# Performance work log

Measured on AMD Instinct MI355X. Metric: run time of the kernel, lower is better.

## Reference

```python
import jax, jax.numpy as jnp
import numpy as np
from jax import lax

DN = ('NCHW', 'OIHW', 'NCHW')


def _conv(x, w, padding, groups=1):
    return lax.conv_general_dilated(
        x, w, window_strides=(1, 1), padding=padding,
        dimension_numbers=DN, feature_group_count=groups)


def _l2_normalize(t, axis=-1, eps=1e-12):
    # matches torch.nn.functional.normalize: x / max(||x||, eps)
    n = jnp.sqrt(jnp.sum(t * t, axis=axis, keepdims=True))
    return t / jnp.maximum(n, eps)


def _topk_masked_softmax(attn, k):
    # attn: [b, H, C, C]; keep exactly the top-k entries per row (by index,
    # matching torch.topk + scatter), set rest to -inf, then softmax.
    C = attn.shape[-1]
    idx = lax.top_k(attn, k)[1]                              # [b, H, C, k]
    mask = jax.nn.one_hot(idx, C, dtype=jnp.bool_).any(-2)   # [b, H, C, C]
    return jax.nn.softmax(jnp.where(mask, attn, -jnp.inf), axis=-1)


def setup_inputs() -> dict:
    key = jax.random.key(0)
    ks = jax.random.split(key, 4)
    dim, heads, b, h, w = 64, 2, 8, 256, 256
    x = jax.random.normal(ks[0], (b, dim, h, w), dtype=jnp.float32)
    w_qkv = jax.random.normal(ks[1], (3 * dim, dim, 1, 1), dtype=jnp.float32) * 0.05
    w_dw = jax.random.normal(ks[2], (3 * dim, 1, 3, 3), dtype=jnp.float32) * 0.05
    w_proj = jax.random.normal(ks[3], (dim, dim, 1, 1), dtype=jnp.float32) * 0.05
    temperature = jnp.ones((heads, 1, 1), dtype=jnp.float32)
    a1 = jnp.array([0.2], dtype=jnp.float32)
    a2 = jnp.array([0.2], dtype=jnp.float32)
    a3 = jnp.array([0.2], dtype=jnp.float32)
    return {"x": x, "w_qkv": w_qkv, "w_dw": w_dw, "w_proj": w_proj,
            "temperature": temperature, "a1": a1, "a2": a2, "a3": a3}


def reference(x, w_qkv, w_dw, w_proj, temperature, a1, a2, a3):
    heads = temperature.shape[0]
    b, c, h, w = x.shape
    qkv = _conv(x, w_qkv, padding=[(0, 0), (0, 0)])
    qkv = _conv(qkv, w_dw, padding=[(1, 1), (1, 1)], groups=3 * c)
    q, k, v = jnp.split(qkv, 3, axis=1)

    def to_heads(t):  # b (head C) h w -> b head C (h w)
        return t.reshape(b, heads, c // heads, h * w)

    q, k, v = to_heads(q), to_heads(k), to_heads(v)
    q = _l2_normalize(q)
    k = _l2_normalize(k)

    C = c // heads
    attn = jnp.einsum('bhcn,bhdn->bhcd', q, k) * temperature  # [b, H, C, C]

    attn1 = _topk_masked_softmax(attn, C // 2)
    attn2 = _topk_masked_softmax(attn, (C * 2) // 3)
    attn3 = _topk_masked_softmax(attn, (C * 3) // 4)

    out = (jnp.einsum('bhcd,bhdn->bhcn', attn1, v) * a1
           + jnp.einsum('bhcd,bhdn->bhcn', attn2, v) * a2
           + jnp.einsum('bhcd,bhdn->bhcn', attn3, v) * a3)

    out = out.reshape(b, c, h, w)
    return _conv(out, w_proj, padding=[(0, 0), (0, 0)])
```

## Files before the change

kernel.cpp:

```cpp
#include <hip/hip_runtime.h>
#include <math.h>

constexpr int B_   = 8;
constexpr int CIN  = 64;
constexpr int C3   = 192;
constexpr int HWID = 256;
constexpr long long NPIX = 65536;

constexpr int K3_CHUNKS = 128;
constexpr int K3_CELLS  = 1088;

constexpr size_t SZ_QKV1_1B = (size_t)C3 * NPIX;
constexpr size_t SZ_QKB_1B  = (size_t)128 * NPIX;
constexpr size_t SZ_GRAM = (size_t)B_ * 2 * 32 * 32;
constexpr size_t SZ_NORM = (size_t)B_ * 2 * 64;
constexpr size_t SZ_M    = (size_t)B_ * 64 * 64;
constexpr size_t SZ_PART = (size_t)B_ * 2 * K3_CHUNKS * K3_CELLS;

constexpr int LSTR = 68;

__global__ __launch_bounds__(256) void k1_qkv1x1(const float* __restrict__ x,
                                                 const float* __restrict__ wqkv,
                                                 float* __restrict__ qkv1, int b0) {
  __shared__ __align__(16) float xs[64][LSTR];
  __shared__ __align__(16) float Wt[64][LSTR];
  const int t = threadIdx.x;
  const int lb = blockIdx.z;
  const long long n0 = (long long)blockIdx.x * 64;
  const int oc0 = blockIdx.y * 64;
  const float* xb = x + (size_t)(b0 + lb) * CIN * NPIX;
  float* outb = qkv1 + (size_t)lb * SZ_QKV1_1B;

  {
    const int p4 = (t & 15) * 4;
#pragma unroll
    for (int r = 0; r < 4; ++r) {
      const int ic = (t >> 4) + 16 * r;
      const float4 v = *(const float4*)(xb + (size_t)ic * NPIX + n0 + p4);
      *(float4*)(&xs[ic][p4]) = v;
    }
    const int ic4 = (t & 15) * 4;
#pragma unroll
    for (int r = 0; r < 4; ++r) {
      const int ocl = (t >> 4) + 16 * r;
      const float4 w = *(const float4*)(wqkv + (size_t)(oc0 + ocl) * 64 + ic4);
      Wt[ic4 + 0][ocl] = w.x;
      Wt[ic4 + 1][ocl] = w.y;
      Wt[ic4 + 2][ocl] = w.z;
      Wt[ic4 + 3][ocl] = w.w;
    }
  }
  __syncthreads();

  const int ocl0 = (t >> 4) * 4;
  const int p0   = (t & 15) * 4;
  float acc[4][4] = {};
#pragma unroll 4
  for (int j = 0; j < 64; ++j) {
    const float4 a  = *(const float4*)(&Wt[j][ocl0]);
    const float4 bq = *(const float4*)(&xs[j][p0]);
    const float av[4] = {a.x, a.y, a.z, a.w};
    const float bv[4] = {bq.x, bq.y, bq.z, bq.w};
#pragma unroll
    for (int i = 0; i < 4; ++i)
#pragma unroll
      for (int p = 0; p < 4; ++p)
        acc[i][p] = fmaf(av[i], bv[p], acc[i][p]);
  }
#pragma unroll
  for (int i = 0; i < 4; ++i) {
    float4 o;
    o.x = acc[i][0]; o.y = acc[i][1]; o.z = acc[i][2]; o.w = acc[i][3];
    *(float4*)(outb + (size_t)(oc0 + ocl0 + i) * NPIX + n0 + p0) = o;
  }
}

__global__ __launch_bounds__(256) void k2_dwconv(const float* __restrict__ qkv1,
                                                 const float* __restrict__ wdw,
                                                 float* __restrict__ qkb,
                                                 size_t qkb_stride,
                                                 float* __restrict__ vout) {
  const int r0 = blockIdx.x * 16;
  const int ch = blockIdx.y;
  const int lb = blockIdx.z;
  const int t  = threadIdx.x;
  __shared__ __align__(16) float sm[18][256];
  const float* p = qkv1 + (size_t)lb * SZ_QKV1_1B + (size_t)ch * NPIX;

  for (int idx = t; idx < 18 * 64; idx += 256) {
    const int rr = idx >> 6;
    const int c4 = (idx & 63) * 4;
    const int gr = r0 - 1 + rr;
    float4 v = make_float4(0.f, 0.f, 0.f, 0.f);
    if (gr >= 0 && gr < HWID) v = *(const float4*)(p + (size_t)gr * HWID + c4);
    *(float4*)(&sm[rr][c4]) = v;
  }
  float w[9];
#pragma unroll
  for (int i = 0; i < 9; ++i) w[i] = wdw[ch * 9 + i];
  __syncthreads();

  const int col = t;
  const bool cl = (col > 0), cr = (col < 255);
  float l0 = cl ? sm[0][col - 1] : 0.f, m0 = sm[0][col], r0v = cr ? sm[0][col + 1] : 0.f;
  float l1 = cl ? sm[1][col - 1] : 0.f, m1 = sm[1][col], r1v = cr ? sm[1][col + 1] : 0.f;
  float* dst = (ch < 128)
                   ? (qkb + (size_t)lb * qkb_stride + (size_t)ch * NPIX)
                   : (vout + (size_t)lb * 64 * NPIX + (size_t)(ch - 128) * NPIX);
#pragma unroll
  for (int k = 0; k < 16; ++k) {
    const float l2 = cl ? sm[k + 2][col - 1] : 0.f;
    const float m2 = sm[k + 2][col];
    const float r2v = cr ? sm[k + 2][col + 1] : 0.f;
    float acc = w[0] * l0;
    acc = fmaf(w[1], m0, acc);  acc = fmaf(w[2], r0v, acc);
    acc = fmaf(w[3], l1, acc);  acc = fmaf(w[4], m1, acc);
    acc = fmaf(w[5], r1v, acc); acc = fmaf(w[6], l2, acc);
    acc = fmaf(w[7], m2, acc);  acc = fmaf(w[8], r2v, acc);
    dst[(size_t)(r0 + k) * HWID + col] = acc;
    l0 = l1; m0 = m1; r0v = r1v;
    l1 = l2; m1 = m2; r1v = r2v;
  }
}

__global__ __launch_bounds__(1024) void k3_gram(const float* __restrict__ qkbuf,
                                                size_t qkb_stride,
                                                float* __restrict__ part, int b0) {
  const int chunk = blockIdx.x;
  const int h = blockIdx.y;
  const int lb = blockIdx.z;
  const int b = b0 + lb;
  const int t = threadIdx.x;
  const int nt = t & 15;
  const int tile = t >> 4;
  const int c0 = (tile & 7) * 4;
  const int d0 = (tile >> 3) * 4;
  const bool do_qn = (d0 == 0);
  const bool do_kn = (c0 == 0);
  const float* base = qkbuf + (size_t)lb * qkb_stride;
  const float* qb = base + (size_t)(h * 32) * NPIX;
  const float* kb = base + (size_t)(64 + h * 32) * NPIX;

  float acc[4][4] = {};
  float qn[4] = {}, kn[4] = {};
  const long long n0 = (long long)chunk * 512 + nt * 4;
#pragma unroll 2
  for (int s = 0; s < 8; ++s) {
    const long long n = n0 + (long long)s * 64;
    float4 qv[4], kv[4];
#pragma unroll
    for (int i = 0; i < 4; ++i)
      qv[i] = *(const float4*)(qb + (size_t)(c0 + i) * NPIX + n);
#pragma unroll
    for (int j = 0; j < 4; ++j)
      kv[j] = *(const float4*)(kb + (size_t)(d0 + j) * NPIX + n);
#pragma unroll
    for (int i = 0; i < 4; ++i)
#pragma unroll
      for (int j = 0; j < 4; ++j) {
        float a = acc[i][j];
        a = fmaf(qv[i].x, kv[j].x, a);
        a = fmaf(qv[i].y, kv[j].y, a);
        a = fmaf(qv[i].z, kv[j].z, a);
        a = fmaf(qv[i].w, kv[j].w, a);
        acc[i][j] = a;
      }
    if (do_qn) {
#pragma unroll
      for (int i = 0; i < 4; ++i) {
        float a = qn[i];
        a = fmaf(qv[i].x, qv[i].x, a);
        a = fmaf(qv[i].y, qv[i].y, a);
        a = fmaf(qv[i].z, qv[i].z, a);
        a = fmaf(qv[i].w, qv[i].w, a);
        qn[i] = a;
      }
    }
    if (do_kn) {
#pragma unroll
      for (int j = 0; j < 4; ++j) {
        float a = kn[j];
        a = fmaf(kv[j].x, kv[j].x, a);
        a = fmaf(kv[j].y, kv[j].y, a);
        a = fmaf(kv[j].z, kv[j].z, a);
        a = fmaf(kv[j].w, kv[j].w, a);
        kn[j] = a;
      }
    }
  }

  float* pb = part + (((size_t)(b * 2 + h)) * K3_CHUNKS + chunk) * K3_CELLS;
#pragma unroll
  for (int i = 0; i < 4; ++i)
#pragma unroll
    for (int j = 0; j < 4; ++j) {
      float v = acc[i][j];
      v += __shfl_xor(v, 1); v += __shfl_xor(v, 2);
      v += __shfl_xor(v, 4); v += __shfl_xor(v, 8);
      if (nt == 0) pb[(c0 + i) * 32 + (d0 + j)] = v;
    }
  if (do_qn) {
#pragma unroll
    for (int i = 0; i < 4; ++i) {
      float v = qn[i];
      v += __shfl_xor(v, 1); v += __shfl_xor(v, 2);
      v += __shfl_xor(v, 4); v += __shfl_xor(v, 8);
      if (nt == 0) pb[1024 + c0 + i] = v;
    }
  }
  if (do_kn) {
#pragma unroll
    for (int j = 0; j < 4; ++j) {
      float v = kn[j];
      v += __shfl_xor(v, 1); v += __shfl_xor(v, 2);
      v += __shfl_xor(v, 4); v += __shfl_xor(v, 8);
      if (nt == 0) pb[1056 + d0 + j] = v;
    }
  }
}

__global__ __launch_bounds__(256) void k3_reduce(const float* __restrict__ part,
                                                 float* __restrict__ gram,
                                                 float* __restrict__ norms) {
  const int e = blockIdx.x * 256 + threadIdx.x;
  const int bh = e / K3_CELLS;
  const int cell = e - bh * K3_CELLS;
  const float* p = part + ((size_t)bh * K3_CHUNKS) * K3_CELLS + cell;
  float s0 = 0.f, s1 = 0.f;
#pragma unroll 4
  for (int ch = 0; ch < K3_CHUNKS; ch += 2) {
    s0 += p[(size_t)ch * K3_CELLS];
    s1 += p[(size_t)(ch + 1) * K3_CELLS];
  }
  const float s = s0 + s1;
  if (cell < 1024) gram[(size_t)bh * 1024 + cell] = s;
  else             norms[(size_t)bh * 64 + (cell - 1024)] = s;
}

__global__ __launch_bounds__(256) void k4_attn(const float* __restrict__ gram,
                                               const float* __restrict__ norms,
                                               const float* __restrict__ temp,
                                               const float* __restrict__ a1,
                                               const float* __restrict__ a2,
                                               const float* __restrict__ a3,
                                               const float* __restrict__ wproj,
                                               float* __restrict__ M) {
  const int b = blockIdx.x;
  const int t = threadIdx.x;
  __shared__ float A[2][32][32];
  if (t < 64) {
    const int h = t >> 5, c = t & 31;
    const float* g = gram + (((size_t)b * 2 + h) * 32 + c) * 32;
    const float* nb = norms + ((size_t)b * 2 + h) * 64;
    const float qn = fmaxf(sqrtf(nb[c]), 1e-12f);
    const float tmph = temp[h];
    float v[32];
#pragma unroll
    for (int d = 0; d < 32; ++d) {
      const float kn = fmaxf(sqrtf(nb[32 + d]), 1e-12f);
      v[d] = g[d] / (qn * kn) * tmph;
    }
    int rank[32];
#pragma unroll
    for (int i = 0; i < 32; ++i) {
      int r = 0;
#pragma unroll
      for (int j = 0; j < 32; ++j)
        r += (v[j] > v[i]) || (v[j] == v[i] && j < i);
      rank[i] = r;
    }
    float acc[32];
#pragma unroll
    for (int d = 0; d < 32; ++d) acc[d] = 0.f;
    const float aws[3] = {a1[0], a2[0], a3[0]};
    const int kvs[3] = {16, 21, 24};
#pragma unroll 1
    for (int kk = 0; kk < 3; ++kk) {
      float mx = -3.4e38f;
#pragma unroll
      for (int d = 0; d < 32; ++d)
        if (rank[d] < kvs[kk]) mx = fmaxf(mx, v[d]);
      float s = 0.f;
#pragma unroll
      for (int d = 0; d < 32; ++d)
        if (rank[d] < kvs[kk]) s += expf(v[d] - mx);
      const float inv = aws[kk] / s;
#pragma unroll
      for (int d = 0; d < 32; ++d)
        if (rank[d] < kvs[kk]) acc[d] += expf(v[d] - mx) * inv;
    }
#pragma unroll
    for (int d = 0; d < 32; ++d) A[h][c][d] = acc[d];
  }
  __syncthreads();
  for (int e = t; e < 4096; e += 256) {
    const int oc = e >> 6, j = e & 63, h = j >> 5, d = j & 31;
    float s = 0.f;
#pragma unroll
    for (int c = 0; c < 32; ++c)
      s += wproj[oc * 64 + h * 32 + c] * A[h][c][d];
    M[(size_t)b * 4096 + e] = s;
  }
}

__global__ __launch_bounds__(256) void k5_out(float* vy,
                                              const float* __restrict__ M) {
  __shared__ __align__(16) float vs[64][LSTR];
  __shared__ __align__(16) float Mt[64][LSTR];
  const int t = threadIdx.x;
  const int b = blockIdx.y;
  const long long n0 = (long long)blockIdx.x * 64;
  float* vb = vy + (size_t)b * 64 * NPIX;
  const float* Mb = M + (size_t)b * 4096;

  {
    const int p4 = (t & 15) * 4;
#pragma unroll
    for (int r = 0; r < 4; ++r) {
      const int j = (t >> 4) + 16 * r;
      const float4 v = *(const float4*)(vb + (size_t)j * NPIX + n0 + p4);
      *(float4*)(&vs[j][p4]) = v;
    }
    const int j4 = (t & 15) * 4;
#pragma unroll
    for (int r = 0; r < 4; ++r) {
      const int oc = (t >> 4) + 16 * r;
      const float4 m = *(const float4*)(Mb + (size_t)oc * 64 + j4);
      Mt[j4 + 0][oc] = m.x;
      Mt[j4 + 1][oc] = m.y;
      Mt[j4 + 2][oc] = m.z;
      Mt[j4 + 3][oc] = m.w;
    }
  }
  __syncthreads();

  const int ocl0 = (t >> 4) * 4;
  const int p0   = (t & 15) * 4;
  float acc[4][4] = {};
#pragma unroll 4
  for (int j = 0; j < 64; ++j) {
    const float4 a  = *(const float4*)(&Mt[j][ocl0]);
    const float4 bq = *(const float4*)(&vs[j][p0]);
    const float av[4] = {a.x, a.y, a.z, a.w};
    const float bv[4] = {bq.x, bq.y, bq.z, bq.w};
#pragma unroll
    for (int i = 0; i < 4; ++i)
#pragma unroll
      for (int p = 0; p < 4; ++p)
        acc[i][p] = fmaf(av[i], bv[p], acc[i][p]);
  }
#pragma unroll
  for (int i = 0; i < 4; ++i) {
    float4 o;
    o.x = acc[i][0]; o.y = acc[i][1]; o.z = acc[i][2]; o.w = acc[i][3];
    *(float4*)(vb + (size_t)(ocl0 + i) * NPIX + n0 + p0) = o;
  }
}

extern "C" void kernel_launch(void* const* d_in, const int* in_sizes, int n_in,
                              void* d_out, int out_size, void* d_ws, size_t ws_size,
                              hipStream_t stream) {
  const float* x     = (const float*)d_in[0];
  const float* wqkv  = (const float*)d_in[1];
  const float* wdw   = (const float*)d_in[2];
  const float* wproj = (const float*)d_in[3];
  const float* temp  = (const float*)d_in[4];
  const float* a1    = (const float*)d_in[5];
  const float* a2    = (const float*)d_in[6];
  const float* a3    = (const float*)d_in[7];
  float* y = (float*)d_out;
  float* ws = (float*)d_ws;

  const size_t ws_floats = ws_size / sizeof(float);
  const size_t smalls = SZ_GRAM + SZ_NORM + SZ_M + SZ_PART;
  const size_t needA = 4 * SZ_QKV1_1B + (size_t)B_ * SZ_QKB_1B + smalls;

  dim3 blk(256);
  if (ws_floats >= needA) {
    float* qkv1  = ws;
    float* qkb   = qkv1 + 4 * SZ_QKV1_1B;
    float* gram  = qkb + (size_t)B_ * SZ_QKB_1B;
    float* norms = gram + SZ_GRAM;
    float* M     = norms + SZ_NORM;
    float* part  = M + SZ_M;

    for (int half = 0; half < 2; ++half) {
      const int b0 = half * 4;
      k1_qkv1x1<<<dim3(1024, 3, 4), blk, 0, stream>>>(x, wqkv, qkv1, b0);
      k2_dwconv<<<dim3(16, C3, 4), blk, 0, stream>>>(
          qkv1, wdw, qkb + (size_t)b0 * SZ_QKB_1B, SZ_QKB_1B,
          y + (size_t)b0 * 64 * NPIX);
    }
    k3_gram<<<dim3(K3_CHUNKS, 2, B_), dim3(1024), 0, stream>>>(
        qkb, SZ_QKB_1B, part, 0);
    k3_reduce<<<dim3(68), blk, 0, stream>>>(part, gram, norms);
    k4_attn<<<dim3(B_), blk, 0, stream>>>(gram, norms, temp, a1, a2, a3, wproj, M);
    k5_out<<<dim3(1024, B_), blk, 0, stream>>>(y, M);
  } else {
    float* qkv1  = ws;
    float* qkb   = qkv1 + SZ_QKV1_1B;
    float* gram  = qkb + SZ_QKB_1B;
    float* norms = gram + SZ_GRAM;
    float* M     = norms + SZ_NORM;
    float* part  = M + SZ_M;

    for (int b = 0; b < B_; ++b) {
      k1_qkv1x1<<<dim3(1024, 3, 1), blk, 0, stream>>>(x, wqkv, qkv1, b);
      k2_dwconv<<<dim3(16, C3, 1), blk, 0, stream>>>(
          qkv1, wdw, qkb, 0, y + (size_t)b * 64 * NPIX);
      k3_gram<<<dim3(K3_CHUNKS, 2, 1), dim3(1024), 0, stream>>>(qkb, 0, part, b);
    }
    k3_reduce<<<dim3(68), blk, 0, stream>>>(part, gram, norms);
    k4_attn<<<dim3(B_), blk, 0, stream>>>(gram, norms, temp, a1, a2, a3, wproj, M);
    k5_out<<<dim3(1024, B_), blk, 0, stream>>>(y, M);
  }
}
```

Measured before the change: 761.8 us.

## Stage Gram tiles in shared memory with 8x8 register blocking and transposed partials

The Gram kernel now loads 32x256 Q and K chunks into shared memory, and each of 256 threads computes an 8x8 output tile instead of reading 4x4 tiles straight from global memory with 1024 threads. This raises arithmetic reuse per load and doubles the chunk count to 256. The partials layout is transposed to cell-major so the reduce kernel can sum each cell's 256 chunks with coalesced loads and a wavefront shuffle. The larger per-thread register tile may lower occupancy, and the partials writes are now strided.

```diff
diff --git a/kernel.cpp b/kernel.cpp
--- a/kernel.cpp
+++ b/kernel.cpp
@@ -7,7 +7,7 @@
 constexpr int HWID = 256;
 constexpr long long NPIX = 65536;
 
-constexpr int K3_CHUNKS = 128;
+constexpr int K3_CHUNKS = 256;
 constexpr int K3_CELLS  = 1088;
 
 constexpr size_t SZ_QKV1_1B = (size_t)C3 * NPIX;
@@ -15,7 +15,7 @@
 constexpr size_t SZ_GRAM = (size_t)B_ * 2 * 32 * 32;
 constexpr size_t SZ_NORM = (size_t)B_ * 2 * 64;
 constexpr size_t SZ_M    = (size_t)B_ * 64 * 64;
-constexpr size_t SZ_PART = (size_t)B_ * 2 * K3_CHUNKS * K3_CELLS;
+constexpr size_t SZ_PART = (size_t)B_ * 2 * K3_CELLS * K3_CHUNKS;
 
 constexpr int LSTR = 68;
 
@@ -123,41 +123,54 @@
   }
 }
 
-__global__ __launch_bounds__(1024) void k3_gram(const float* __restrict__ qkbuf,
-                                                size_t qkb_stride,
-                                                float* __restrict__ part, int b0) {
+__global__ __launch_bounds__(256) void k3_gram(const float* __restrict__ qkbuf,
+                                               size_t qkb_stride,
+                                               float* __restrict__ part, int b0) {
+  constexpr int LS = 260;
+  __shared__ __align__(16) float qs[32][LS];
+  __shared__ __align__(16) float ks[32][LS];
   const int chunk = blockIdx.x;
   const int h = blockIdx.y;
   const int lb = blockIdx.z;
   const int b = b0 + lb;
   const int t = threadIdx.x;
+  const float* base = qkbuf + (size_t)lb * qkb_stride;
+  const float* qg = base + (size_t)(h * 32) * NPIX + (size_t)chunk * 256;
+  const float* kg = base + (size_t)(64 + h * 32) * NPIX + (size_t)chunk * 256;
+
+  {
+    const int col4 = (t & 63) * 4;
+    const int rb = t >> 6;
+#pragma unroll
+    for (int it = 0; it < 8; ++it) {
+      const int row = it * 4 + rb;
+      *(float4*)(&qs[row][col4]) = *(const float4*)(qg + (size_t)row * NPIX + col4);
+      *(float4*)(&ks[row][col4]) = *(const float4*)(kg + (size_t)row * NPIX + col4);
+    }
+  }
+  __syncthreads();
+
   const int nt = t & 15;
   const int tile = t >> 4;
-  const int c0 = (tile & 7) * 4;
-  const int d0 = (tile >> 3) * 4;
+  const int c0 = (tile & 3) * 8;
+  const int d0 = (tile >> 2) * 8;
   const bool do_qn = (d0 == 0);
   const bool do_kn = (c0 == 0);
-  const float* base = qkbuf + (size_t)lb * qkb_stride;
-  const float* qb = base + (size_t)(h * 32) * NPIX;
-  const float* kb = base + (size_t)(64 + h * 32) * NPIX;
-
-  float acc[4][4] = {};
-  float qn[4] = {}, kn[4] = {};
-  const long long n0 = (long long)chunk * 512 + nt * 4;
-#pragma unroll 2
-  for (int s = 0; s < 8; ++s) {
-    const long long n = n0 + (long long)s * 64;
-    float4 qv[4], kv[4];
-#pragma unroll
-    for (int i = 0; i < 4; ++i)
-      qv[i] = *(const float4*)(qb + (size_t)(c0 + i) * NPIX + n);
-#pragma unroll
-    for (int j = 0; j < 4; ++j)
-      kv[j] = *(const float4*)(kb + (size_t)(d0 + j) * NPIX + n);
-#pragma unroll
-    for (int i = 0; i < 4; ++i)
-#pragma unroll
-      for (int j = 0; j < 4; ++j) {
+
+  float acc[8][8] = {};
+  float qn[8] = {}, kn[8] = {};
+#pragma unroll 1
+  for (int s = 0; s < 4; ++s) {
+    const int nn = s * 64 + nt * 4;
+    float4 qv[8], kv[8];
+#pragma unroll
+    for (int i = 0; i < 8; ++i) qv[i] = *(const float4*)(&qs[c0 + i][nn]);
+#pragma unroll
+    for (int j = 0; j < 8; ++j) kv[j] = *(const float4*)(&ks[d0 + j][nn]);
+#pragma unroll
+    for (int i = 0; i < 8; ++i)
+#pragma unroll
+      for (int j = 0; j < 8; ++j) {
         float a = acc[i][j];
         a = fmaf(qv[i].x, kv[j].x, a);
         a = fmaf(qv[i].y, kv[j].y, a);
@@ -167,7 +180,7 @@
       }
     if (do_qn) {
 #pragma unroll
-      for (int i = 0; i < 4; ++i) {
+      for (int i = 0; i < 8; ++i) {
         float a = qn[i];
         a = fmaf(qv[i].x, qv[i].x, a);
         a = fmaf(qv[i].y, qv[i].y, a);
@@ -178,7 +191,7 @@
     }
     if (do_kn) {
 #pragma unroll
-      for (int j = 0; j < 4; ++j) {
+      for (int j = 0; j < 8; ++j) {
         float a = kn[j];
         a = fmaf(kv[j].x, kv[j].x, a);
         a = fmaf(kv[j].y, kv[j].y, a);
@@ -189,32 +202,32 @@
     }
   }
 
-  float* pb = part + (((size_t)(b * 2 + h)) * K3_CHUNKS + chunk) * K3_CELLS;
-#pragma unroll
-  for (int i = 0; i < 4; ++i)
-#pragma unroll
-    for (int j = 0; j < 4; ++j) {
+  float* pb = part + ((size_t)(b * 2 + h) * K3_CELLS) * K3_CHUNKS + chunk;
+#pragma unroll
+  for (int i = 0; i < 8; ++i)
+#pragma unroll
+    for (int j = 0; j < 8; ++j) {
       float v = acc[i][j];
       v += __shfl_xor(v, 1); v += __shfl_xor(v, 2);
       v += __shfl_xor(v, 4); v += __shfl_xor(v, 8);
-      if (nt == 0) pb[(c0 + i) * 32 + (d0 + j)] = v;
+      if (nt == 0) pb[(size_t)((c0 + i) * 32 + (d0 + j)) * K3_CHUNKS] = v;
     }
   if (do_qn) {
 #pragma unroll
-    for (int i = 0; i < 4; ++i) {
+    for (int i = 0; i < 8; ++i) {
       float v = qn[i];
       v += __shfl_xor(v, 1); v += __shfl_xor(v, 2);
       v += __shfl_xor(v, 4); v += __shfl_xor(v, 8);
-      if (nt == 0) pb[1024 + c0 + i] = v;
+      if (nt == 0) pb[(size_t)(1024 + c0 + i) * K3_CHUNKS] = v;
     }
   }
   if (do_kn) {
 #pragma unroll
-    for (int j = 0; j < 4; ++j) {
+    for (int j = 0; j < 8; ++j) {
       float v = kn[j];
       v += __shfl_xor(v, 1); v += __shfl_xor(v, 2);
       v += __shfl_xor(v, 4); v += __shfl_xor(v, 8);
-      if (nt == 0) pb[1056 + d0 + j] = v;
+      if (nt == 0) pb[(size_t)(1056 + d0 + j) * K3_CHUNKS] = v;
     }
   }
 }
@@ -222,19 +235,20 @@
 __global__ __launch_bounds__(256) void k3_reduce(const float* __restrict__ part,
                                                  float* __restrict__ gram,
                                                  float* __restrict__ norms) {
-  const int e = blockIdx.x * 256 + threadIdx.x;
-  const int bh = e / K3_CELLS;
-  const int cell = e - bh * K3_CELLS;
-  const float* p = part + ((size_t)bh * K3_CHUNKS) * K3_CELLS + cell;
-  float s0 = 0.f, s1 = 0.f;
-#pragma unroll 4
-  for (int ch = 0; ch < K3_CHUNKS; ch += 2) {
-    s0 += p[(size_t)ch * K3_CELLS];
-    s1 += p[(size_t)(ch + 1) * K3_CELLS];
-  }
-  const float s = s0 + s1;
-  if (cell < 1024) gram[(size_t)bh * 1024 + cell] = s;
-  else             norms[(size_t)bh * 64 + (cell - 1024)] = s;
+  const int t = threadIdx.x;
+  const int e = blockIdx.x * 4 + (t >> 6);
+  const int l = t & 63;
+  const float* p = part + (size_t)e * K3_CHUNKS;
+  float s = p[l] + p[l + 64] + p[l + 128] + p[l + 192];
+  s += __shfl_xor(s, 1);  s += __shfl_xor(s, 2);
+  s += __shfl_xor(s, 4);  s += __shfl_xor(s, 8);
+  s += __shfl_xor(s, 16); s += __shfl_xor(s, 32);
+  if (l == 0) {
+    const int bh = e / K3_CELLS;
+    const int cell = e - bh * K3_CELLS;
+    if (cell < 1024) gram[(size_t)bh * 1024 + cell] = s;
+    else             norms[(size_t)bh * 64 + (cell - 1024)] = s;
+  }
 }
 
 __global__ __launch_bounds__(256) void k4_attn(const float* __restrict__ gram,
@@ -391,9 +405,9 @@
           qkv1, wdw, qkb + (size_t)b0 * SZ_QKB_1B, SZ_QKB_1B,
           y + (size_t)b0 * 64 * NPIX);
     }
-    k3_gram<<<dim3(K3_CHUNKS, 2, B_), dim3(1024), 0, stream>>>(
+    k3_gram<<<dim3(K3_CHUNKS, 2, B_), blk, 0, stream>>>(
         qkb, SZ_QKB_1B, part, 0);
-    k3_reduce<<<dim3(68), blk, 0, stream>>>(part, gram, norms);
+    k3_reduce<<<dim3(4352), blk, 0, stream>>>(part, gram, norms);
     k4_attn<<<dim3(B_), blk, 0, stream>>>(gram, norms, temp, a1, a2, a3, wproj, M);
     k5_out<<<dim3(1024, B_), blk, 0, stream>>>(y, M);
   } else {
@@ -408,9 +422,9 @@
       k1_qkv1x1<<<dim3(1024, 3, 1), blk, 0, stream>>>(x, wqkv, qkv1, b);
       k2_dwconv<<<dim3(16, C3, 1), blk, 0, stream>>>(
           qkv1, wdw, qkb, 0, y + (size_t)b * 64 * NPIX);
-      k3_gram<<<dim3(K3_CHUNKS, 2, 1), dim3(1024), 0, stream>>>(qkb, 0, part, b);
-    }
-    k3_reduce<<<dim3(68), blk, 0, stream>>>(part, gram, norms);
+      k3_gram<<<dim3(K3_CHUNKS, 2, 1), blk, 0, stream>>>(qkb, 0, part, b);
+    }
+    k3_reduce<<<dim3(4352), blk, 0, stream>>>(part, gram, norms);
     k4_attn<<<dim3(B_), blk, 0, stream>>>(gram, norms, temp, a1, a2, a3, wproj, M);
     k5_out<<<dim3(1024, B_), blk, 0, stream>>>(y, M);
   }
```

Measured after the change: 751.6 us. About the same (-1.3%).
